# Optimization experiments

Hardware: AMD Instinct MI355X
Metric: run time of the kernel (lower is better)

Reference implementation:

```python
import jax, jax.numpy as jnp
import numpy as np

D_MODEL = 256
N_HEAD = 8


def quick_gelu(x):
    return x * jax.nn.sigmoid(1.702 * x)


def setup_inputs() -> dict:
    key = jax.random.key(0)
    ks = jax.random.split(key, 7)
    d = D_MODEL
    s = 0.02
    return {
        "x": jax.random.normal(ks[0], (2, 512, d), dtype=jnp.float32),
        "W_qkv": jax.random.normal(ks[1], (d, 3 * d), dtype=jnp.float32) * s,
        "b_qkv": jnp.zeros((3 * d,), dtype=jnp.float32),
        "W_fc": jax.random.normal(ks[2], (d, 4 * d), dtype=jnp.float32) * s,
        "b_fc": jnp.zeros((4 * d,), dtype=jnp.float32),
        "W_proj": jax.random.normal(ks[3], (4 * d, d), dtype=jnp.float32) * s,
        "b_proj": jnp.zeros((d,), dtype=jnp.float32),
    }


def attention_l1(x, W_qkv, b_qkv):
    bs, n_ctx, width = x.shape
    h = N_HEAD
    c = width // h
    scale = 1.0 / jnp.sqrt(jnp.asarray(c, x.dtype))
    qkv = (x @ W_qkv + b_qkv).reshape(bs, n_ctx, h, 3 * c)
    q, k, v = jnp.split(qkv, 3, axis=-1)  # each (b, t, h, c)
    qh = q.transpose(0, 2, 1, 3)  # (b, h, t, c)
    kh = k.transpose(0, 2, 1, 3)  # (b, h, s, c)
    vh = v.transpose(0, 2, 1, 3)  # (b, h, s, c)
    # L1 distance: sum_c |q - k| * scale  -> (b, h, t, s)
    dist = jnp.sum(jnp.abs(qh[:, :, :, None, :] - kh[:, :, None, :, :]), axis=-1) * scale
    weight = 1.0 / (0.001 + dist)
    idx = jnp.arange(n_ctx)
    weight = weight.at[:, :, idx, idx].set(0.0)
    wdtype = weight.dtype
    weight = jax.nn.softmax(weight.astype(jnp.float32), axis=-1).astype(wdtype)
    out = jnp.einsum('bhts,bhsc->bthc', weight, vh)
    return out.reshape(bs, n_ctx, width)


def reference(x, W_qkv, b_qkv, W_fc, b_fc, W_proj, b_proj):
    x = x + attention_l1(x, W_qkv, b_qkv)
    h = quick_gelu(x @ W_fc + b_fc)
    x = x + (h @ W_proj + b_proj)
    return x
```

## Files before the change

kernel.cpp:

```cpp
#include <hip/hip_runtime.h>
#include <hip/hip_bf16.h>
#include <hip/hip_fp16.h>

#define DM   256
#define NH   8
#define HC   32
#define SEQ  512
#define MTOT 1024

#define B_X1   0
#define B_QH   (1u<<20)
#define B_KH   0x180000u
#define B_VT   0x200000u
#define B_WFCT 0x280000u
#define B_WPJT 0x300000u

typedef __attribute__((ext_vector_type(8))) __bf16 bf16x8;
typedef __attribute__((ext_vector_type(4))) __bf16 bf16x4;
typedef __attribute__((ext_vector_type(4))) float  f32x4;

__device__ __forceinline__ float qgelu(float x) {
    return x / (1.0f + __expf(-1.702f * x));
}

__global__ __launch_bounds__(256)
void qkv_k(const float* __restrict__ x, const float* __restrict__ W,
           const float* __restrict__ bias,
           const float* __restrict__ Wfc, const float* __restrict__ Wproj,
           char* __restrict__ wsb)
{
    __shared__ float lt[64 * 65];
    const int bid = blockIdx.x, tid = threadIdx.x;

    if (bid >= 768) {
        const int tt = bid - 768;
        const float* src; __bf16* dst; int K, N, tile;
        if (tt < 64) { src = Wfc;   dst = (__bf16*)(wsb + B_WFCT); K = 256;  N = 1024; tile = tt; }
        else         { src = Wproj; dst = (__bf16*)(wsb + B_WPJT); K = 1024; N = 256;  tile = tt - 64; }
        const int nn = N >> 6;
        const int k0 = (tile / nn) * 64, n0 = (tile % nn) * 64;
        const int rr0 = tid >> 4, c4 = tid & 15;
        #pragma unroll
        for (int i = 0; i < 4; ++i) {
            const int rr = rr0 + i * 16;
            float4 v = *(const float4*)&src[(size_t)(k0 + rr) * N + n0 + c4 * 4];
            lt[rr * 65 + c4 * 4 + 0] = v.x; lt[rr * 65 + c4 * 4 + 1] = v.y;
            lt[rr * 65 + c4 * 4 + 2] = v.z; lt[rr * 65 + c4 * 4 + 3] = v.w;
        }
        __syncthreads();
        #pragma unroll
        for (int i = 0; i < 4; ++i) {
            const int rr = rr0 + i * 16;
            bf16x4 b;
            b.x = (__bf16)lt[(c4 * 4 + 0) * 65 + rr];
            b.y = (__bf16)lt[(c4 * 4 + 1) * 65 + rr];
            b.z = (__bf16)lt[(c4 * 4 + 2) * 65 + rr];
            b.w = (__bf16)lt[(c4 * 4 + 3) * 65 + rr];
            *(bf16x4*)&dst[(size_t)(n0 + rr) * K + k0 + c4 * 4] = b;
        }
        return;
    }

    const int lane = tid & 63, wv = tid >> 6;
    const int widx = bid * 4 + wv;
    const int m0 = (widx & 63) * 16, n0 = (widx >> 6) * 16;
    const int r = lane & 15, q = lane >> 4;

    const float* ap = x + (size_t)(m0 + r) * DM + q * 8;
    const float* bp = W + (size_t)(q * 8) * 768 + n0 + r;

    f32x4 acc = {0.f, 0.f, 0.f, 0.f};
    #pragma unroll
    for (int kt = 0; kt < DM; kt += 32) {
        float4 a0 = *(const float4*)(ap + kt);
        float4 a1 = *(const float4*)(ap + kt + 4);
        bf16x8 af;
        af[0] = (__bf16)a0.x; af[1] = (__bf16)a0.y; af[2] = (__bf16)a0.z; af[3] = (__bf16)a0.w;
        af[4] = (__bf16)a1.x; af[5] = (__bf16)a1.y; af[6] = (__bf16)a1.z; af[7] = (__bf16)a1.w;
        bf16x8 bf;
        #pragma unroll
        for (int j = 0; j < 8; ++j)
            bf[j] = (__bf16)bp[(size_t)(kt + j) * 768];
        acc = __builtin_amdgcn_mfma_f32_16x16x32_bf16(af, bf, acc, 0, 0, 0);
    }

    __half*  qh  = (__half*)(wsb + B_QH);
    __half*  kh  = (__half*)(wsb + B_KH);
    __bf16*  vtb = (__bf16*)(wsb + B_VT);
    const int n = n0 + r;
    const float bn = bias[n];
    const int h = n / 96, jj = n % 96;
    #pragma unroll
    for (int i = 0; i < 4; ++i) {
        const int m = m0 + q * 4 + i;
        const float v = acc[i] + bn;
        const int b = m >> 9, t = m & 511;
        const int bh = b * NH + h;
        if (jj < 32)      qh[((size_t)(bh * SEQ + t)) * HC + jj]        = (__half)v;
        else if (jj < 64) kh[((size_t)(bh * SEQ + t)) * HC + (jj - 32)] = (__half)v;
        else              vtb[((size_t)(bh * HC + (jj - 64))) * SEQ + t] = (__bf16)v;
    }
}

#define QT 16
#define PSTRIDE 514

__global__ __launch_bounds__(512, 4)
void attn_k(const char* __restrict__ wsb, const float* __restrict__ xin,
            float* __restrict__ x1)
{
    __shared__ __half2 qtile[QT * 16];
    __shared__ __bf16  pmat[QT * PSTRIDE];
    __shared__ float   psum[QT * 8];
    __shared__ float   pinv[QT];

    const __half*  qhg = (const __half*)(wsb + B_QH);
    const __half*  khg = (const __half*)(wsb + B_KH);
    const __bf16*  vtb = (const __bf16*)(wsb + B_VT);

    const int tid  = threadIdx.x;
    const int lane = tid & 63;
    const int wv   = tid >> 6;
    const int sg   = tid;
    const int bh   = blockIdx.x >> 5;
    const int qbase = (blockIdx.x & 31) * QT;
    const float scale = 0.17677669529663687f;

    const __half2* kp = (const __half2*)(khg + ((size_t)(bh * SEQ + sg)) * HC);
    __half2 kr[16];
    #pragma unroll
    for (int j = 0; j < 16; ++j) kr[j] = kp[j];

    if (tid < 256) {
        const int t = tid >> 4, j = tid & 15;
        qtile[t * 16 + j] =
            *(const __half2*)(qhg + ((size_t)(bh * SEQ + qbase + t)) * HC + j * 2);
    }
    __syncthreads();

    #pragma unroll 4
    for (int t = 0; t < QT; ++t) {
        __half2 acc2 = __floats2half2_rn(0.f, 0.f);
        #pragma unroll
        for (int j = 0; j < 16; ++j) {
            __half2 dif = __hsub2(kr[j], qtile[t * 16 + j]);
            unsigned u = (*(unsigned*)&dif) & 0x7FFF7FFFu;
            acc2 = __hadd2(acc2, *(__half2*)&u);
        }
        const float d = __low2float(acc2) + __high2float(acc2);
        float w = 1.0f / (0.001f + d * scale);
        if (sg == qbase + t) w = 0.0f;
        float p = __expf(w);
        float se = p;
        #pragma unroll
        for (int off = 32; off >= 1; off >>= 1) se += __shfl_xor(se, off, 64);
        pmat[t * PSTRIDE + sg] = (__bf16)p;
        if (lane == 0) psum[t * 8 + wv] = se;
    }
    __syncthreads();

    if (tid < QT) {
        float s = 0.f;
        #pragma unroll
        for (int j = 0; j < 8; ++j) s += psum[tid * 8 + j];
        pinv[tid] = 1.0f / s;
    }
    __syncthreads();

    if (wv < 2) {
        const int r = lane & 15, q = lane >> 4;
        const __bf16* bp  = vtb + ((size_t)(bh * HC + wv * 16 + r)) * SEQ + q * 8;
        const __bf16* apm = &pmat[r * PSTRIDE + q * 8];
        f32x4 acc = {0.f, 0.f, 0.f, 0.f};
        #pragma unroll
        for (int kt = 0; kt < SEQ; kt += 32) {
            bf16x8 af = *(const bf16x8*)(apm + kt);
            bf16x8 bf = *(const bf16x8*)(bp + kt);
            acc = __builtin_amdgcn_mfma_f32_16x16x32_bf16(af, bf, acc, 0, 0, 0);
        }
        const int b = bh >> 3, hh = bh & 7;
        const int c = wv * 16 + r;
        #pragma unroll
        for (int i = 0; i < 4; ++i) {
            const int tl = q * 4 + i;
            const int t  = qbase + tl;
            const float v = acc[i] * pinv[tl];
            const int idx = ((b * SEQ + t) * DM) + hh * HC + c;
            x1[idx] = xin[idx] + v;
        }
    }
}

#define HSTR 1032

__global__ __launch_bounds__(512)
void mlp_k(const float* __restrict__ X1, const char* __restrict__ wsb,
           const float* __restrict__ bfc, const float* __restrict__ bproj,
           float* __restrict__ out)
{
    __shared__ __bf16 hl[16 * HSTR];
    const __bf16* Wf = (const __bf16*)(wsb + B_WFCT);
    const __bf16* Wp = (const __bf16*)(wsb + B_WPJT);

    const int tid  = threadIdx.x;
    const int lane = tid & 63;
    const int wv   = tid >> 6;
    const int m0   = blockIdx.x * 16;
    const int r    = lane & 15, q = lane >> 4;

    {
        const float* ap = X1 + (size_t)(m0 + r) * DM + q * 8;
        f32x4 acc[8] = {};
        #pragma unroll
        for (int kt = 0; kt < DM; kt += 32) {
            float4 a0 = *(const float4*)(ap + kt);
            float4 a1 = *(const float4*)(ap + kt + 4);
            bf16x8 af;
            af[0] = (__bf16)a0.x; af[1] = (__bf16)a0.y; af[2] = (__bf16)a0.z; af[3] = (__bf16)a0.w;
            af[4] = (__bf16)a1.x; af[5] = (__bf16)a1.y; af[6] = (__bf16)a1.z; af[7] = (__bf16)a1.w;
            #pragma unroll
            for (int nt = 0; nt < 8; ++nt) {
                const int n0 = (wv * 8 + nt) * 16;
                bf16x8 bf = *(const bf16x8*)(Wf + (size_t)(n0 + r) * DM + q * 8 + kt);
                acc[nt] = __builtin_amdgcn_mfma_f32_16x16x32_bf16(af, bf, acc[nt], 0, 0, 0);
            }
        }
        #pragma unroll
        for (int nt = 0; nt < 8; ++nt) {
            const int n = (wv * 8 + nt) * 16 + r;
            const float bn = bfc[n];
            #pragma unroll
            for (int i = 0; i < 4; ++i)
                hl[(q * 4 + i) * HSTR + n] = (__bf16)qgelu(acc[nt][i] + bn);
        }
    }
    __syncthreads();

    {
        f32x4 acc[2] = {};
        const __bf16* al = &hl[r * HSTR + q * 8];
        #pragma unroll 4
        for (int kt = 0; kt < 1024; kt += 32) {
            bf16x8 af = *(const bf16x8*)(al + kt);
            #pragma unroll
            for (int nt = 0; nt < 2; ++nt) {
                const int n0 = (wv * 2 + nt) * 16;
                bf16x8 bf = *(const bf16x8*)(Wp + (size_t)(n0 + r) * 1024 + q * 8 + kt);
                acc[nt] = __builtin_amdgcn_mfma_f32_16x16x32_bf16(af, bf, acc[nt], 0, 0, 0);
            }
        }
        #pragma unroll
        for (int nt = 0; nt < 2; ++nt) {
            const int n = (wv * 2 + nt) * 16 + r;
            const float bn = bproj[n];
            #pragma unroll
            for (int i = 0; i < 4; ++i) {
                const int m = m0 + q * 4 + i;
                out[(size_t)m * DM + n] =
                    X1[(size_t)m * DM + n] + acc[nt][i] + bn;
            }
        }
    }
}

extern "C" void kernel_launch(void* const* d_in, const int* in_sizes, int n_in,
                              void* d_out, int out_size, void* d_ws, size_t ws_size,
                              hipStream_t stream)
{
    (void)in_sizes; (void)n_in; (void)out_size; (void)ws_size;
    const float* x     = (const float*)d_in[0];
    const float* Wqkv  = (const float*)d_in[1];
    const float* bqkv  = (const float*)d_in[2];
    const float* Wfc   = (const float*)d_in[3];
    const float* bfc   = (const float*)d_in[4];
    const float* Wproj = (const float*)d_in[5];
    const float* bproj = (const float*)d_in[6];
    float* out = (float*)d_out;
    char*  wsb = (char*)d_ws;
    float* x1  = (float*)(wsb + B_X1);

    qkv_k<<<896, 256, 0, stream>>>(x, Wqkv, bqkv, Wfc, Wproj, wsb);

    attn_k<<<512, 512, 0, stream>>>(wsb, x, x1);

    mlp_k<<<64, 512, 0, stream>>>(x1, wsb, bfc, bproj, out);
}
```

Measured before the change: 126.8 us.

## Split MLP hidden dimension across blocks with atomic accumulation into output

The MLP kernel is split along the 1024-wide hidden dimension into four 256-wide slices. Launch grows from 64 blocks of 512 threads to 256 blocks of 256 threads, each computing a partial down-projection and adding it into the output with float atomics. The attention kernel now pre-initialises the output with the residual plus the projection bias so the partial sums can accumulate on top of it. This raises parallelism on a GPU that was underfilled with 64 blocks, at the cost of atomic traffic and non-deterministic summation order.

```diff
diff --git a/kernel.cpp b/kernel.cpp
--- a/kernel.cpp
+++ b/kernel.cpp
@@ -107,7 +107,8 @@
 
 __global__ __launch_bounds__(512, 4)
 void attn_k(const char* __restrict__ wsb, const float* __restrict__ xin,
-            float* __restrict__ x1)
+            float* __restrict__ x1, const float* __restrict__ bproj,
+            float* __restrict__ out)
 {
     __shared__ __half2 qtile[QT * 16];
     __shared__ __bf16  pmat[QT * PSTRIDE];
@@ -180,37 +181,42 @@
         }
         const int b = bh >> 3, hh = bh & 7;
         const int c = wv * 16 + r;
+        const int col = hh * HC + c;
+        const float bpn = bproj[col];
         #pragma unroll
         for (int i = 0; i < 4; ++i) {
             const int tl = q * 4 + i;
             const int t  = qbase + tl;
             const float v = acc[i] * pinv[tl];
-            const int idx = ((b * SEQ + t) * DM) + hh * HC + c;
-            x1[idx] = xin[idx] + v;
-        }
-    }
-}
-
-#define HSTR 1032
-
-__global__ __launch_bounds__(512)
+            const int idx = ((b * SEQ + t) * DM) + col;
+            const float res = xin[idx] + v;
+            x1[idx]  = res;
+            out[idx] = res + bpn;
+        }
+    }
+}
+
+#define HSTR 264
+
+__global__ __launch_bounds__(256)
 void mlp_k(const float* __restrict__ X1, const char* __restrict__ wsb,
-           const float* __restrict__ bfc, const float* __restrict__ bproj,
-           float* __restrict__ out)
-{
-    __shared__ __bf16 hl[16 * HSTR];
+           const float* __restrict__ bfc, float* __restrict__ out)
+{
+    __shared__ __bf16 hs[16 * HSTR];
     const __bf16* Wf = (const __bf16*)(wsb + B_WFCT);
     const __bf16* Wp = (const __bf16*)(wsb + B_WPJT);
 
     const int tid  = threadIdx.x;
     const int lane = tid & 63;
     const int wv   = tid >> 6;
-    const int m0   = blockIdx.x * 16;
+    const int mt   = blockIdx.x & 63;
+    const int ns   = blockIdx.x >> 6;
+    const int m0   = mt * 16;
     const int r    = lane & 15, q = lane >> 4;
 
     {
         const float* ap = X1 + (size_t)(m0 + r) * DM + q * 8;
-        f32x4 acc[8] = {};
+        f32x4 acc[4] = {};
         #pragma unroll
         for (int kt = 0; kt < DM; kt += 32) {
             float4 a0 = *(const float4*)(ap + kt);
@@ -219,45 +225,44 @@
             af[0] = (__bf16)a0.x; af[1] = (__bf16)a0.y; af[2] = (__bf16)a0.z; af[3] = (__bf16)a0.w;
             af[4] = (__bf16)a1.x; af[5] = (__bf16)a1.y; af[6] = (__bf16)a1.z; af[7] = (__bf16)a1.w;
             #pragma unroll
-            for (int nt = 0; nt < 8; ++nt) {
-                const int n0 = (wv * 8 + nt) * 16;
+            for (int nt = 0; nt < 4; ++nt) {
+                const int n0 = ns * 256 + (wv * 4 + nt) * 16;
                 bf16x8 bf = *(const bf16x8*)(Wf + (size_t)(n0 + r) * DM + q * 8 + kt);
                 acc[nt] = __builtin_amdgcn_mfma_f32_16x16x32_bf16(af, bf, acc[nt], 0, 0, 0);
             }
         }
         #pragma unroll
-        for (int nt = 0; nt < 8; ++nt) {
-            const int n = (wv * 8 + nt) * 16 + r;
-            const float bn = bfc[n];
+        for (int nt = 0; nt < 4; ++nt) {
+            const int nl = (wv * 4 + nt) * 16 + r;
+            const float bn = bfc[ns * 256 + nl];
             #pragma unroll
             for (int i = 0; i < 4; ++i)
-                hl[(q * 4 + i) * HSTR + n] = (__bf16)qgelu(acc[nt][i] + bn);
+                hs[(q * 4 + i) * HSTR + nl] = (__bf16)qgelu(acc[nt][i] + bn);
         }
     }
     __syncthreads();
 
     {
-        f32x4 acc[2] = {};
-        const __bf16* al = &hl[r * HSTR + q * 8];
-        #pragma unroll 4
-        for (int kt = 0; kt < 1024; kt += 32) {
+        f32x4 acc[4] = {};
+        const __bf16* al = &hs[r * HSTR + q * 8];
+        #pragma unroll
+        for (int kt = 0; kt < 256; kt += 32) {
             bf16x8 af = *(const bf16x8*)(al + kt);
             #pragma unroll
-            for (int nt = 0; nt < 2; ++nt) {
-                const int n0 = (wv * 2 + nt) * 16;
-                bf16x8 bf = *(const bf16x8*)(Wp + (size_t)(n0 + r) * 1024 + q * 8 + kt);
+            for (int nt = 0; nt < 4; ++nt) {
+                const int n0 = wv * 64 + nt * 16;
+                bf16x8 bf = *(const bf16x8*)(Wp + (size_t)(n0 + r) * 1024 +
+                                             ns * 256 + q * 8 + kt);
                 acc[nt] = __builtin_amdgcn_mfma_f32_16x16x32_bf16(af, bf, acc[nt], 0, 0, 0);
             }
         }
         #pragma unroll
-        for (int nt = 0; nt < 2; ++nt) {
-            const int n = (wv * 2 + nt) * 16 + r;
-            const float bn = bproj[n];
+        for (int nt = 0; nt < 4; ++nt) {
+            const int n = wv * 64 + nt * 16 + r;
             #pragma unroll
             for (int i = 0; i < 4; ++i) {
                 const int m = m0 + q * 4 + i;
-                out[(size_t)m * DM + n] =
-                    X1[(size_t)m * DM + n] + acc[nt][i] + bn;
+                atomicAdd(&out[(size_t)m * DM + n], acc[nt][i]);
             }
         }
     }
@@ -281,7 +286,7 @@
 
     qkv_k<<<896, 256, 0, stream>>>(x, Wqkv, bqkv, Wfc, Wproj, wsb);
 
-    attn_k<<<512, 512, 0, stream>>>(wsb, x, x1);
-
-    mlp_k<<<64, 512, 0, stream>>>(x1, wsb, bfc, bproj, out);
-}
+    attn_k<<<512, 512, 0, stream>>>(wsb, x, x1, bproj, out);
+
+    mlp_k<<<256, 256, 0, stream>>>(x1, wsb, bfc, out);
+}
```

After: 106.3 us, median of 2. 1.19x faster.
